# Kernel tuning notes

Measured on AMD Instinct MI355X. Metric: run time of the kernel, lower is better.

Reference implementation:

```python
import jax, jax.numpy as jnp
import numpy as np

B = 524288

def setup_inputs() -> dict:
    key = jax.random.key(0)
    ks = jax.random.split(key, 9)
    return {
        "x":  jax.random.uniform(ks[0], (B, 1, 9, 9), dtype=jnp.float32),
        "Wc": jax.random.normal(ks[1], (81, 9), dtype=jnp.float32),
        "bc": jax.random.normal(ks[2], (81,), dtype=jnp.float32),
        "Wh": jax.random.normal(ks[3], (27, 9), dtype=jnp.float32),
        "bh": jax.random.normal(ks[4], (27,), dtype=jnp.float32),
        "Wm": jax.random.normal(ks[5], (12, 9), dtype=jnp.float32),
        "bm": jax.random.normal(ks[6], (12,), dtype=jnp.float32),
        "Wo": jax.random.normal(ks[7], (4, 4), dtype=jnp.float32),
        "bo": jax.random.normal(ks[8], (4,), dtype=jnp.float32),
    }

def _forward(x, Wc, bc, Wh, bh, Wm, bm, Wo, bo):
    b = x.shape[0]
    # 9 non-overlapping 3x3 patches (stride 3 over 9x9): (B, 9 patches, 9 pixels)
    p = x[:, 0].reshape(b, 3, 3, 3, 3).transpose(0, 1, 3, 2, 4).reshape(b, 9, 9)
    # conv layer: 9 logic kernels per patch -> (B, 9, 9) -> (B, 81)
    feat = jax.nn.sigmoid(
        jnp.einsum('bgp,gkp->bgk', p, Wc.reshape(9, 9, 9)) + bc.reshape(9, 9)
    ).reshape(b, 81)
    # hidden layer: 9 groups x 3 neurons, each over 9 inputs -> (B, 27)
    h = jax.nn.sigmoid(
        jnp.einsum('bgp,gnp->bgn', feat.reshape(b, 9, 9), Wh.reshape(9, 3, 9))
        + bh.reshape(9, 3)
    ).reshape(b, 27)
    # middle layer: 3 groups x 4 neurons, each over 9 inputs -> (B, 12)
    m = jax.nn.sigmoid(
        jnp.einsum('bgp,gnp->bgn', h.reshape(b, 3, 9), Wm.reshape(3, 4, 9))
        + bm.reshape(3, 4)
    ).reshape(b, 12)
    # output layer: class c reads middle group c % 3 (4 values each)
    num_classes = Wo.shape[0]
    grp = jnp.arange(num_classes) % 3                   # (C,)
    mg = m.reshape(b, 3, 4)[:, grp]                     # (B, C, 4)
    output_logits = jnp.einsum('bcp,cp->bc', mg, Wo) + bo
    return output_logits

def reference(x, Wc, bc, Wh, bh, Wm, bm, Wo, bo):
    return _forward(x, Wc, bc, Wh, bh, Wm, bm, Wo, bo)
```

## Files before the change

### kernel.cpp

```cpp
#include <hip/hip_runtime.h>

#define THREADS 256
#define SAMPLES_PER_BLOCK 512

__device__ __forceinline__ float fast_sigmoid(float v) {
    float e = __expf(-v);
    return __builtin_amdgcn_rcpf(1.0f + e);
}

__global__ __launch_bounds__(THREADS) void olcnn_kernel(
    const float* __restrict__ x,
    const float* __restrict__ Wc, const float* __restrict__ bc,
    const float* __restrict__ Wh, const float* __restrict__ bh,
    const float* __restrict__ Wm, const float* __restrict__ bm,
    const float* __restrict__ Wo, const float* __restrict__ bo,
    float* __restrict__ out)
{
    const int tid  = threadIdx.x;
    const int wave = tid >> 6, lane = tid & 63;
    const int s0 = blockIdx.x * SAMPLES_PER_BLOCK + wave * 128 + lane;
    const int s1 = s0 + 64;

    const float* xA = x + s0 * 81;
    const float* xB = x + s1 * 81;

    float res[2][4];

    #pragma unroll
    for (int G = 0; G < 3; ++G) {
        float c0[27], c1[27];
        #pragma unroll
        for (int j = 0; j < 27; ++j) c0[j] = xA[G * 27 + j];
        #pragma unroll
        for (int j = 0; j < 27; ++j) c1[j] = xB[G * 27 + j];

        float hb0[9], hb1[9];
        #pragma unroll
        for (int j = 0; j < 3; ++j) {
            const int g = G * 3 + j;
            float ft0[9], ft1[9];
            #pragma unroll
            for (int k = 0; k < 9; ++k) {
                float a0 = bc[g * 9 + k], a1 = a0;
                #pragma unroll
                for (int pr = 0; pr < 3; ++pr)
                    #pragma unroll
                    for (int pc = 0; pc < 3; ++pc) {
                        const float w = Wc[(g * 9 + k) * 9 + pr * 3 + pc];
                        const int ci = pr * 9 + j * 3 + pc;
                        a0 = fmaf(c0[ci], w, a0);
                        a1 = fmaf(c1[ci], w, a1);
                    }
                ft0[k] = fast_sigmoid(a0);
                ft1[k] = fast_sigmoid(a1);
            }
            #pragma unroll
            for (int n = 0; n < 3; ++n) {
                float a0 = bh[g * 3 + n], a1 = a0;
                #pragma unroll
                for (int p = 0; p < 9; ++p) {
                    const float w = Wh[(g * 3 + n) * 9 + p];
                    a0 = fmaf(ft0[p], w, a0);
                    a1 = fmaf(ft1[p], w, a1);
                }
                hb0[j * 3 + n] = fast_sigmoid(a0);
                hb1[j * 3 + n] = fast_sigmoid(a1);
            }
        }

        float m0[4], m1[4];
        #pragma unroll
        for (int n = 0; n < 4; ++n) {
            float a0 = bm[G * 4 + n], a1 = a0;
            #pragma unroll
            for (int p = 0; p < 9; ++p) {
                const float w = Wm[(G * 4 + n) * 9 + p];
                a0 = fmaf(hb0[p], w, a0);
                a1 = fmaf(hb1[p], w, a1);
            }
            m0[n] = fast_sigmoid(a0);
            m1[n] = fast_sigmoid(a1);
        }

        {
            float a0 = bo[G], a1 = a0;
            #pragma unroll
            for (int p = 0; p < 4; ++p) {
                const float w = Wo[G * 4 + p];
                a0 = fmaf(m0[p], w, a0);
                a1 = fmaf(m1[p], w, a1);
            }
            res[0][G] = a0; res[1][G] = a1;
        }
        if (G == 0) {
            float a0 = bo[3], a1 = a0;
            #pragma unroll
            for (int p = 0; p < 4; ++p) {
                const float w = Wo[3 * 4 + p];
                a0 = fmaf(m0[p], w, a0);
                a1 = fmaf(m1[p], w, a1);
            }
            res[0][3] = a0; res[1][3] = a1;
        }
    }

    float4 o0, o1;
    o0.x = res[0][0]; o0.y = res[0][1]; o0.z = res[0][2]; o0.w = res[0][3];
    o1.x = res[1][0]; o1.y = res[1][1]; o1.z = res[1][2]; o1.w = res[1][3];
    ((float4*)out)[s0] = o0;
    ((float4*)out)[s1] = o1;
}

extern "C" void kernel_launch(void* const* d_in, const int* in_sizes, int n_in,
                              void* d_out, int out_size, void* d_ws, size_t ws_size,
                              hipStream_t stream) {
    const float* x  = (const float*)d_in[0];
    const float* Wc = (const float*)d_in[1];
    const float* bc = (const float*)d_in[2];
    const float* Wh = (const float*)d_in[3];
    const float* bh = (const float*)d_in[4];
    const float* Wm = (const float*)d_in[5];
    const float* bm = (const float*)d_in[6];
    const float* Wo = (const float*)d_in[7];
    const float* bo = (const float*)d_in[8];
    float* out = (float*)d_out;

    const int B = in_sizes[0] / 81;
    const int blocks = B / SAMPLES_PER_BLOCK;
    olcnn_kernel<<<blocks, THREADS, 0, stream>>>(x, Wc, bc, Wh, bh, Wm, bm,
                                                 Wo, bo, out);
}
```

Before: 285.4 us.

## Roll group loops and stream the middle layer to cut register pressure

```diff
diff --git a/kernel.cpp b/kernel.cpp
--- a/kernel.cpp
+++ b/kernel.cpp
@@ -1,7 +1,8 @@
 #include <hip/hip_runtime.h>
 
 #define THREADS 256
-#define SAMPLES_PER_BLOCK 512
+#define SPT 2
+#define SAMPLES_PER_BLOCK (THREADS * SPT)
 
 __device__ __forceinline__ float fast_sigmoid(float v) {
     float e = __expf(-v);
@@ -18,97 +19,97 @@
 {
     const int tid  = threadIdx.x;
     const int wave = tid >> 6, lane = tid & 63;
-    const int s0 = blockIdx.x * SAMPLES_PER_BLOCK + wave * 128 + lane;
+    const int s0 = blockIdx.x * SAMPLES_PER_BLOCK + wave * (64 * SPT) + lane;
     const int s1 = s0 + 64;
-
     const float* xA = x + s0 * 81;
     const float* xB = x + s1 * 81;
 
-    float res[2][4];
+    float rA0 = 0.f, rA1 = 0.f, rA2 = 0.f, rA3 = 0.f;
+    float rB0 = 0.f, rB1 = 0.f, rB2 = 0.f, rB3 = 0.f;
 
-    #pragma unroll
+    #pragma clang loop unroll(disable)
     for (int G = 0; G < 3; ++G) {
-        float c0[27], c1[27];
+        float mA[4], mB[4];
         #pragma unroll
-        for (int j = 0; j < 27; ++j) c0[j] = xA[G * 27 + j];
-        #pragma unroll
-        for (int j = 0; j < 27; ++j) c1[j] = xB[G * 27 + j];
+        for (int n4 = 0; n4 < 4; ++n4) { mA[n4] = bm[G * 4 + n4]; mB[n4] = mA[n4]; }
 
-        float hb0[9], hb1[9];
-        #pragma unroll
+        #pragma clang loop unroll(disable)
         for (int j = 0; j < 3; ++j) {
             const int g = G * 3 + j;
-            float ft0[9], ft1[9];
+            const float* wc = Wc + g * 81;
+
+            float p0[9], p1[9];
+            #pragma unroll
+            for (int pr = 0; pr < 3; ++pr)
+                #pragma unroll
+                for (int pc = 0; pc < 3; ++pc) {
+                    const int off = G * 27 + pr * 9 + j * 3 + pc;
+                    p0[pr * 3 + pc] = xA[off];
+                    p1[pr * 3 + pc] = xB[off];
+                }
+
+            float f0[9], f1[9];
             #pragma unroll
             for (int k = 0; k < 9; ++k) {
                 float a0 = bc[g * 9 + k], a1 = a0;
                 #pragma unroll
-                for (int pr = 0; pr < 3; ++pr)
-                    #pragma unroll
-                    for (int pc = 0; pc < 3; ++pc) {
-                        const float w = Wc[(g * 9 + k) * 9 + pr * 3 + pc];
-                        const int ci = pr * 9 + j * 3 + pc;
-                        a0 = fmaf(c0[ci], w, a0);
-                        a1 = fmaf(c1[ci], w, a1);
-                    }
-                ft0[k] = fast_sigmoid(a0);
-                ft1[k] = fast_sigmoid(a1);
+                for (int p = 0; p < 9; ++p) {
+                    const float w = wc[k * 9 + p];
+                    a0 = fmaf(p0[p], w, a0);
+                    a1 = fmaf(p1[p], w, a1);
+                }
+                f0[k] = fast_sigmoid(a0);
+                f1[k] = fast_sigmoid(a1);
             }
+
             #pragma unroll
             for (int n = 0; n < 3; ++n) {
                 float a0 = bh[g * 3 + n], a1 = a0;
                 #pragma unroll
                 for (int p = 0; p < 9; ++p) {
                     const float w = Wh[(g * 3 + n) * 9 + p];
-                    a0 = fmaf(ft0[p], w, a0);
-                    a1 = fmaf(ft1[p], w, a1);
+                    a0 = fmaf(f0[p], w, a0);
+                    a1 = fmaf(f1[p], w, a1);
                 }
-                hb0[j * 3 + n] = fast_sigmoid(a0);
-                hb1[j * 3 + n] = fast_sigmoid(a1);
+                const float h0 = fast_sigmoid(a0);
+                const float h1 = fast_sigmoid(a1);
+                #pragma unroll
+                for (int n4 = 0; n4 < 4; ++n4) {
+                    const float w = Wm[(G * 4 + n4) * 9 + j * 3 + n];
+                    mA[n4] = fmaf(h0, w, mA[n4]);
+                    mB[n4] = fmaf(h1, w, mB[n4]);
+                }
             }
         }
 
-        float m0[4], m1[4];
         #pragma unroll
-        for (int n = 0; n < 4; ++n) {
-            float a0 = bm[G * 4 + n], a1 = a0;
-            #pragma unroll
-            for (int p = 0; p < 9; ++p) {
-                const float w = Wm[(G * 4 + n) * 9 + p];
-                a0 = fmaf(hb0[p], w, a0);
-                a1 = fmaf(hb1[p], w, a1);
-            }
-            m0[n] = fast_sigmoid(a0);
-            m1[n] = fast_sigmoid(a1);
+        for (int n4 = 0; n4 < 4; ++n4) {
+            mA[n4] = fast_sigmoid(mA[n4]);
+            mB[n4] = fast_sigmoid(mB[n4]);
         }
 
-        {
-            float a0 = bo[G], a1 = a0;
-            #pragma unroll
-            for (int p = 0; p < 4; ++p) {
-                const float w = Wo[G * 4 + p];
-                a0 = fmaf(m0[p], w, a0);
-                a1 = fmaf(m1[p], w, a1);
-            }
-            res[0][G] = a0; res[1][G] = a1;
+        float oA = bo[G], oB = oA;
+        float qA = bo[3], qB = qA;
+        #pragma unroll
+        for (int p = 0; p < 4; ++p) {
+            const float wg = Wo[G * 4 + p];
+            const float w3 = Wo[12 + p];
+            oA = fmaf(mA[p], wg, oA);
+            oB = fmaf(mB[p], wg, oB);
+            qA = fmaf(mA[p], w3, qA);
+            qB = fmaf(mB[p], w3, qB);
         }
-        if (G == 0) {
-            float a0 = bo[3], a1 = a0;
-            #pragma unroll
-            for (int p = 0; p < 4; ++p) {
-                const float w = Wo[3 * 4 + p];
-                a0 = fmaf(m0[p], w, a0);
-                a1 = fmaf(m1[p], w, a1);
-            }
-            res[0][3] = a0; res[1][3] = a1;
-        }
+        rA0 = (G == 0) ? oA : rA0;  rB0 = (G == 0) ? oB : rB0;
+        rA1 = (G == 1) ? oA : rA1;  rB1 = (G == 1) ? oB : rB1;
+        rA2 = (G == 2) ? oA : rA2;  rB2 = (G == 2) ? oB : rB2;
+        rA3 = (G == 0) ? qA : rA3;  rB3 = (G == 0) ? qB : rB3;
     }
 
-    float4 o0, o1;
-    o0.x = res[0][0]; o0.y = res[0][1]; o0.z = res[0][2]; o0.w = res[0][3];
-    o1.x = res[1][0]; o1.y = res[1][1]; o1.z = res[1][2]; o1.w = res[1][3];
-    ((float4*)out)[s0] = o0;
-    ((float4*)out)[s1] = o1;
+    float4 oA4, oB4;
+    oA4.x = rA0; oA4.y = rA1; oA4.z = rA2; oA4.w = rA3;
+    oB4.x = rB0; oB4.y = rB1; oB4.z = rB2; oB4.w = rB3;
+    ((float4*)out)[s0] = oA4;
+    ((float4*)out)[s1] = oB4;
 }
 
 extern "C" void kernel_launch(void* const* d_in, const int* in_sizes, int n_in,
```

New measurement: 328.1 us. +15.0%, slower.
